# Performance work log

Hardware: AMD Instinct MI355X
Metric: run time of the kernel (lower is better)

Reference implementation:

```python
import jax, jax.numpy as jnp
import numpy as np

N, C, L, K = 8, 128, 1024, 100   # batch, channels, encoded seq len, num_negatives
TEMP = 0.5                        # contrastive temperature
EPS = 1e-8                        # cosine-similarity norm clamp (torch default)


def setup_inputs() -> dict:
    key = jax.random.key(0)
    kz, kc, kn = jax.random.split(key, 3)
    z = jax.random.normal(kz, (N, C, L), dtype=jnp.float32)
    c = jax.random.normal(kc, (N, C, L + 1), dtype=jnp.float32)
    # Uniform sampling of K distinct indices per (n, l), excluding l itself:
    # equivalent to torch.multinomial(ones(L,L)-eye(L), K) per row, per sample.
    noise = jax.random.uniform(kn, (N, L, L), dtype=jnp.float32)
    noise = noise - 2.0 * jnp.eye(L, dtype=jnp.float32)  # push self-index below everything
    _, neg_inds = jax.lax.top_k(noise, K)                # (N, L, K) int32, distinct, != l
    return {"z": z, "c": c, "neg_inds": neg_inds.astype(jnp.int32)}


def reference(z, c, neg_inds):
    # z: (N, C, L) unmasked convencoder features; c: (N, C, L+1) transformer out
    n, ch, l = z.shape
    z_seq = jnp.transpose(z, (0, 2, 1))                  # (N, L, C)
    # gather negatives: (N, L, K, C)
    negatives = z_seq[jnp.arange(n)[:, None, None], neg_inds]
    # drop start token, move to (N, L, 1, C)
    c_seq = jnp.transpose(c[..., 1:], (0, 2, 1))[:, :, None, :]
    z_tgt = z_seq[:, :, None, :]                         # (N, L, 1, C)
    targets = jnp.concatenate([z_tgt, negatives], axis=2)  # (N, L, K+1, C)
    # cosine similarity along C with torch-style eps clamping
    dot = jnp.sum(c_seq * targets, axis=-1)              # (N, L, K+1)
    c_norm = jnp.maximum(jnp.sqrt(jnp.sum(c_seq * c_seq, axis=-1)), EPS)
    t_norm = jnp.maximum(jnp.sqrt(jnp.sum(targets * targets, axis=-1)), EPS)
    logits = dot / (c_norm * t_norm) / TEMP              # (N, L, K+1)
    # mask negatives that exactly equal the context vector
    neg_in_tgt = jnp.all(c_seq == negatives, axis=-1)    # (N, L, K)
    neg_logits = jnp.where(neg_in_tgt, -jnp.inf, logits[:, :, 1:])
    logits = jnp.concatenate([logits[:, :, :1], neg_logits], axis=2)
    return logits.reshape(-1, K + 1)                     # (N*L, K+1)
```

## Files before the change

kernel.cpp:

```cpp
#include <hip/hip_runtime.h>
#include <math.h>

#define N 8
#define C 128
#define L 1024
#define K 100
#define TEMP 0.5f
#define EPS 1e-8f
#define NT (N * L)

typedef _Float16 half8 __attribute__((ext_vector_type(8)));
typedef float f32x4 __attribute__((ext_vector_type(4)));


__global__ void __launch_bounds__(512)
transpose_frag(const float* __restrict__ z, const float* __restrict__ c,
               half8* __restrict__ zf, half8* __restrict__ cf,
               float* __restrict__ zp, float* __restrict__ cp) {
    __shared__ float tile[64][65];
    __shared__ float part[8][64];
    const int which = blockIdx.z >> 3;
    const int n = blockIdx.z & 7;
    const float* src = which ? c : z;
    half8* dst = which ? cf : zf;
    float* pdst = which ? cp : zp;
    const int slen = which ? (L + 1) : L;
    const int off = which;
    const int l0 = blockIdx.x * 64;
    const int c0 = blockIdx.y * 64;
    const int tx = threadIdx.x;
    const int ty = threadIdx.y;
#pragma unroll
    for (int i = 0; i < 8; i++) {
        int chn = c0 + ty + i * 8;
        tile[ty + i * 8][tx] = src[((size_t)(n * C + chn)) * slen + off + l0 + tx];
    }
    __syncthreads();
    float p = 0.f;
    half8 hv;
#pragma unroll
    for (int q = 0; q < 8; q++) {
        float v = tile[ty * 8 + q][tx];
        p += v * v;
        hv[q] = (_Float16)v;
    }
    const int l = l0 + tx;
    const int ch = c0 + ty * 8;
    const int ks = ch >> 5, kg = (ch >> 3) & 3;
    dst[(((size_t)(n * 64 + (l >> 4)) * 4 + ks) << 6) + (l & 15) + (kg << 4)] = hv;
    part[ty][tx] = p;
    __syncthreads();
    if (ty == 0) {
        float sm = 0.f;
#pragma unroll
        for (int i = 0; i < 8; i++) sm += part[i][tx];
        pdst[(((size_t)n << 10) + l0 + tx) * 2 + (c0 >> 6)] = sm;
    }
}

__global__ void __launch_bounds__(512)
gemm_gather(const half8* __restrict__ zf, const half8* __restrict__ cf,
            const int* __restrict__ neg_inds,
            const float* __restrict__ zp, const float* __restrict__ cp,
            const float* __restrict__ z_orig, const float* __restrict__ c_orig,
            float* __restrict__ out) {
    __shared__ float dotL[16 * L];
    __shared__ float2 zpl[L];
    const int tid  = threadIdx.x;
    const int lane = tid & 63;
    const int w    = tid >> 6;
    const int n    = blockIdx.x >> 6;
    const int tA   = blockIdx.x & 63;

    const float2* zp2 = (const float2*)zp + ((size_t)n << 10);
    for (int i = tid; i < L; i += 512) zpl[i] = zp2[i];

    const size_t nbase = (size_t)n << 14;
    half8 a[4];
#pragma unroll
    for (int ks = 0; ks < 4; ks++)
        a[ks] = cf[nbase + (((tA << 2) + ks) << 6) + lane];

    f32x4 acc[8];
#pragma unroll
    for (int i = 0; i < 8; i++)
#pragma unroll
        for (int r = 0; r < 4; r++) acc[i][r] = 0.f;

#pragma unroll
    for (int ks = 0; ks < 4; ks++) {
#pragma unroll
        for (int nt = 0; nt < 8; nt++) {
            const half8 b = zf[nbase + ((size_t)(((w << 3) + nt) * 4 + ks) << 6) + lane];
            acc[nt] = __builtin_amdgcn_mfma_f32_16x16x32_f16(a[ks], b, acc[nt], 0, 0, 0);
        }
    }

    const int r16 = lane & 15;
    const int kg  = lane >> 4;
#pragma unroll
    for (int nt = 0; nt < 8; nt++)
#pragma unroll
        for (int r = 0; r < 4; r++) {
            const int row = (kg << 2) + r;
            const int col = (((w << 3) + nt) << 4) + r16;
            dotL[(row << 10) + (col ^ (row << 1))] = acc[nt][r];
        }
    __syncthreads();

    const int row = tid >> 5;
    const int sub = tid & 31;
    const int t   = (tA << 4) + row;
    const int ntg = (n << 10) + t;
    const float2 cpv = ((const float2*)cp)[ntg];
    const float cn = cpv.x + cpv.y;
    const float rs_c = 2.0f * rsqrtf(fmaxf(cn, EPS * EPS));
    const int* ni = neg_inds + (size_t)ntg * K;
    float* orow = out + (size_t)ntg * (K + 1);

    for (int kk = sub; kk <= K; kk += 32) {
        const int col = (kk == 0) ? t : ni[kk - 1];
        const float dot = dotL[(row << 10) + (col ^ (row << 1))];
        const float2 tv = zpl[col];
        const float tn = tv.x + tv.y;
        float logit = dot * rs_c * rsqrtf(fmaxf(tn, EPS * EPS));
        if (kk > 0) {
            const float ds = cn - 2.f * dot + tn;
            if (ds < 0.05f * cn) {
                bool eq = true;
                for (int q = 0; q < C; q++) {
                    float cv = c_orig[((size_t)(n * C + q)) * (L + 1) + t + 1];
                    float zv = z_orig[((size_t)(n * C + q)) * L + col];
                    eq = eq && (cv == zv);
                }
                if (eq) logit = -INFINITY;
            }
        }
        orow[kk] = logit;
    }
}

extern "C" void kernel_launch(void* const* d_in, const int* in_sizes, int n_in,
                              void* d_out, int out_size, void* d_ws, size_t ws_size,
                              hipStream_t stream) {
    const float* z   = (const float*)d_in[0];
    const float* c   = (const float*)d_in[1];
    const int*   neg = (const int*)d_in[2];
    float* out = (float*)d_out;

    half8* zf = (half8*)d_ws;
    half8* cf = zf + (size_t)N * 16384;
    float* zp = (float*)(cf + (size_t)N * 16384);
    float* cp = zp + (size_t)NT * 2;

    transpose_frag<<<dim3(L / 64, C / 64, 16), dim3(64, 8), 0, stream>>>(z, c, zf, cf, zp, cp);
    gemm_gather<<<dim3(N * (L / 16)), 512, 0, stream>>>(zf, cf, neg, zp, cp, z, c, out);
}
```

Before: 77.14 us.

## Compute 32 rows per block with fp16 LDS dot cache and B-fragment reuse

Each gemm_gather block now handles 32 query rows instead of 16, reusing each loaded z fragment across two MFMA row tiles. This halves the redundant B loads and the block count. The dot-product staging buffer in LDS is stored as fp16 to fit twice the rows in the same space, and the XOR swizzle is dropped. Launch bounds request two blocks per CU. Rounding the dot to fp16 before normalization adds precision error, and the unswizzled LDS layout may cause bank conflicts.

```diff
diff --git a/kernel.cpp b/kernel.cpp
--- a/kernel.cpp
+++ b/kernel.cpp
@@ -8,6 +8,7 @@
 #define TEMP 0.5f
 #define EPS 1e-8f
 #define NT (N * L)
+#define ROWS 32
 
 typedef _Float16 half8 __attribute__((ext_vector_type(8)));
 typedef float f32x4 __attribute__((ext_vector_type(4)));
@@ -58,59 +59,68 @@
     }
 }
 
-__global__ void __launch_bounds__(512)
+__global__ void __launch_bounds__(512, 2)
 gemm_gather(const half8* __restrict__ zf, const half8* __restrict__ cf,
             const int* __restrict__ neg_inds,
             const float* __restrict__ zp, const float* __restrict__ cp,
             const float* __restrict__ z_orig, const float* __restrict__ c_orig,
             float* __restrict__ out) {
-    __shared__ float dotL[16 * L];
+    __shared__ _Float16 dotH[ROWS * L];
     __shared__ float2 zpl[L];
     const int tid  = threadIdx.x;
     const int lane = tid & 63;
     const int w    = tid >> 6;
-    const int n    = blockIdx.x >> 6;
-    const int tA   = blockIdx.x & 63;
+    const int n    = blockIdx.x >> 5;
+    const int tA   = blockIdx.x & 31;
 
     const float2* zp2 = (const float2*)zp + ((size_t)n << 10);
     for (int i = tid; i < L; i += 512) zpl[i] = zp2[i];
 
     const size_t nbase = (size_t)n << 14;
-    half8 a[4];
+    half8 a[2][4];
 #pragma unroll
-    for (int ks = 0; ks < 4; ks++)
-        a[ks] = cf[nbase + (((tA << 2) + ks) << 6) + lane];
+    for (int at = 0; at < 2; at++)
+#pragma unroll
+        for (int ks = 0; ks < 4; ks++)
+            a[at][ks] = cf[nbase + ((((tA << 1) + at) * 4 + ks) << 6) + lane];
 
-    f32x4 acc[8];
+    f32x4 acc[2][8];
 #pragma unroll
-    for (int i = 0; i < 8; i++)
+    for (int at = 0; at < 2; at++)
 #pragma unroll
-        for (int r = 0; r < 4; r++) acc[i][r] = 0.f;
+        for (int i = 0; i < 8; i++)
+#pragma unroll
+            for (int r = 0; r < 4; r++) acc[at][i][r] = 0.f;
 
 #pragma unroll
     for (int ks = 0; ks < 4; ks++) {
+        half8 b[8];
 #pragma unroll
-        for (int nt = 0; nt < 8; nt++) {
-            const half8 b = zf[nbase + ((size_t)(((w << 3) + nt) * 4 + ks) << 6) + lane];
-            acc[nt] = __builtin_amdgcn_mfma_f32_16x16x32_f16(a[ks], b, acc[nt], 0, 0, 0);
-        }
+        for (int nt = 0; nt < 8; nt++)
+            b[nt] = zf[nbase + ((size_t)(((w << 3) + nt) * 4 + ks) << 6) + lane];
+#pragma unroll
+        for (int nt = 0; nt < 8; nt++)
+            acc[0][nt] = __builtin_amdgcn_mfma_f32_16x16x32_f16(a[0][ks], b[nt], acc[0][nt], 0, 0, 0);
+#pragma unroll
+        for (int nt = 0; nt < 8; nt++)
+            acc[1][nt] = __builtin_amdgcn_mfma_f32_16x16x32_f16(a[1][ks], b[nt], acc[1][nt], 0, 0, 0);
     }
 
     const int r16 = lane & 15;
     const int kg  = lane >> 4;
 #pragma unroll
-    for (int nt = 0; nt < 8; nt++)
+    for (int at = 0; at < 2; at++)
 #pragma unroll
-        for (int r = 0; r < 4; r++) {
-            const int row = (kg << 2) + r;
-            const int col = (((w << 3) + nt) << 4) + r16;
-            dotL[(row << 10) + (col ^ (row << 1))] = acc[nt][r];
-        }
+        for (int nt = 0; nt < 8; nt++)
+#pragma unroll
+            for (int r = 0; r < 4; r++)
+                dotH[((at << 4) + (kg << 2) + r) * L + (w << 7) + (nt << 4) + r16]
+                    = (_Float16)acc[at][nt][r];
     __syncthreads();
 
-    const int row = tid >> 5;
-    const int sub = tid & 31;
-    const int t   = (tA << 4) + row;
+    const int row = tid >> 4;
+    const int sub = tid & 15;
+    const int t   = (tA << 5) + row;
     const int ntg = (n << 10) + t;
     const float2 cpv = ((const float2*)cp)[ntg];
     const float cn = cpv.x + cpv.y;
@@ -118,9 +128,9 @@
     const int* ni = neg_inds + (size_t)ntg * K;
     float* orow = out + (size_t)ntg * (K + 1);
 
-    for (int kk = sub; kk <= K; kk += 32) {
+    for (int kk = sub; kk <= K; kk += 16) {
         const int col = (kk == 0) ? t : ni[kk - 1];
-        const float dot = dotL[(row << 10) + (col ^ (row << 1))];
+        const float dot = (float)dotH[row * L + col];
         const float2 tv = zpl[col];
         const float tn = tv.x + tv.y;
         float logit = dot * rs_c * rsqrtf(fmaxf(tn, EPS * EPS));
@@ -154,5 +164,5 @@
     float* cp = zp + (size_t)NT * 2;
 
     transpose_frag<<<dim3(L / 64, C / 64, 16), dim3(64, 8), 0, stream>>>(z, c, zf, cf, zp, cp);
-    gemm_gather<<<dim3(N * (L / 16)), 512, 0, stream>>>(zf, cf, neg, zp, cp, z, c, out);
+    gemm_gather<<<dim3(N * (L / ROWS)), 512, 0, stream>>>(zf, cf, neg, zp, cp, z, c, out);
 }
```

Result: no change. 76.28 us (-1.1%).
